# Performance work log

Hardware: AMD Instinct MI355X
Metric: run time of the kernel (lower is better)

Reference implementation:

```python
import jax, jax.numpy as jnp
import numpy as np

TOPK = 2


def setup_inputs() -> dict:
    key = jax.random.key(0)
    k1, k2, k3, k4, k5 = jax.random.split(key, 5)
    D, H, E = 1024, 1408, 8
    hidden_states = jax.random.normal(k1, (2, 1024, D), dtype=jnp.float32)
    gate_w = jax.random.normal(k2, (E, D), dtype=jnp.float32) * 0.02
    w1g = jax.random.normal(k3, (E, D, H), dtype=jnp.float32) * 0.02
    w1u = jax.random.normal(k4, (E, D, H), dtype=jnp.float32) * 0.02
    w2 = jax.random.normal(k5, (E, H, D), dtype=jnp.float32) * 0.02
    return {"hidden_states": hidden_states, "gate_w": gate_w, "w1g": w1g, "w1u": w1u, "w2": w2}


def reference(hidden_states, gate_w, w1g, w1u, w2):
    # hidden_states: [B, S, D]; expert weights: w1g/w1u [E, D, H], w2 [E, H, D]
    B, S, D = hidden_states.shape
    E = gate_w.shape[0]
    x = hidden_states.reshape(-1, D)  # [T, D]
    T = x.shape[0]

    # --- MoEGate: softmax scores, top-k routing (no topk renorm) ---
    logits = x @ gate_w.T                      # [T, E]
    scores = jax.nn.softmax(logits, axis=-1)   # [T, E]
    topk_w, topk_idx = jax.lax.top_k(scores, TOPK)  # [T, K]

    # Per-token combine coefficient for each expert: coeff[t, e] = sum_k w[t,k] * (idx[t,k]==e)
    coeff = jnp.zeros((T, E), dtype=x.dtype).at[jnp.arange(T)[:, None], topk_idx].add(topk_w)

    # --- Grouped expert MLP (swiglu): identical math to permute + grouped GEMM + unpermute ---
    g = jnp.einsum('td,edh->teh', x, w1g)      # [T, E, H]
    u = jnp.einsum('td,edh->teh', x, w1u)      # [T, E, H]
    h = jax.nn.silu(g) * u                     # [T, E, H]
    y = jnp.einsum('teh,te,ehd->td', h, coeff, w2)  # [T, D]
    return y.reshape(B, S, D)
```

## Files before the change

### kernel.cpp

```cpp
#include <hip/hip_runtime.h>

#define TOK 2048
#define DDIM 1024
#define HDIM 1408
#define ENUM 8
#define NSLOT (2 * TOK)
#define UP_NB 22
#define UP_KS 32
#define DN_NB 16
#define DN_KS 44
#define DN_KH 22
#define TC_W1_BLK 2816
#define TC_ALL_BLK 4224

typedef unsigned int uint;
typedef unsigned short ushort;

using bf16x8 = __attribute__((ext_vector_type(8))) __bf16;
using f32x4  = __attribute__((ext_vector_type(4))) float;

__device__ __forceinline__ float silu_f(float g) {
    return g / (1.0f + __expf(-g));
}

__device__ __forceinline__ ushort cvt_bf16(float f) {
    uint u = __float_as_uint(f);
    u += 0x7FFFu + ((u >> 16) & 1u);
    return (ushort)(u >> 16);
}

__device__ __forceinline__ void gl2lds16(const void* g, void* l) {
    __builtin_amdgcn_global_load_lds(
        (const __attribute__((address_space(1))) uint*)g,
        (__attribute__((address_space(3))) uint*)l, 16, 0, 0);
}

__global__ __launch_bounds__(64) void gate1_kernel(
    const float* __restrict__ x, const float* __restrict__ gw,
    int* __restrict__ tinfo, float* __restrict__ wslot, ushort* __restrict__ xb)
{
    const int t = blockIdx.x;
    const int lane = threadIdx.x;
    const float* xr = x + (size_t)t * DDIM;
    ushort* xbr = xb + (size_t)t * DDIM;
    float xv[16];
#pragma unroll
    for (int i = 0; i < 16; ++i) xv[i] = xr[lane + 64 * i];
#pragma unroll
    for (int i = 0; i < 16; ++i) xbr[lane + 64 * i] = cvt_bf16(xv[i]);
    float logit[ENUM];
#pragma unroll
    for (int e = 0; e < ENUM; ++e) {
        const float* gr = gw + (size_t)e * DDIM;
        float acc = 0.f;
#pragma unroll
        for (int i = 0; i < 16; ++i) acc += xv[i] * gr[lane + 64 * i];
#pragma unroll
        for (int s = 32; s > 0; s >>= 1) acc += __shfl_xor(acc, s, 64);
        logit[e] = acc;
    }
    if (lane == 0) {
        float mx = logit[0];
#pragma unroll
        for (int e = 1; e < ENUM; ++e) mx = fmaxf(mx, logit[e]);
        float p[ENUM]; float se = 0.f;
#pragma unroll
        for (int e = 0; e < ENUM; ++e) { p[e] = __expf(logit[e] - mx); se += p[e]; }
        float inv = 1.0f / se;
#pragma unroll
        for (int e = 0; e < ENUM; ++e) p[e] *= inv;
        int i0 = 0;
#pragma unroll
        for (int e = 1; e < ENUM; ++e) if (p[e] > p[i0]) i0 = e;
        int i1 = (i0 == 0) ? 1 : 0;
#pragma unroll
        for (int e = 0; e < ENUM; ++e) if (e != i0 && p[e] > p[i1]) i1 = e;
        tinfo[t] = i0 | (i1 << 4);
        wslot[(t << 1)] = p[i0];
        wslot[(t << 1) | 1] = p[i1];
    }
}

__global__ __launch_bounds__(256) void tcast_all_kernel(
    const float* __restrict__ w1g, const float* __restrict__ w1u,
    const float* __restrict__ w2, ushort* __restrict__ BgP,
    ushort* __restrict__ BuP, ushort* __restrict__ W2P,
    const int* __restrict__ tinfo, int* __restrict__ counts,
    int* __restrict__ toks)
{
    const int bid = blockIdx.x;
    const int tid = threadIdx.x;

    __shared__ float Ls[32][69];
    __shared__ int cnt;

    if (bid >= TC_ALL_BLK) {
        const int e = bid - TC_ALL_BLK;
        if (tid == 0) cnt = 0;
        __syncthreads();
        for (int t = tid; t < TOK; t += 256) {
            int info = tinfo[t];
            if ((info & 15) == e) { int p = atomicAdd(&cnt, 1); toks[e * TOK + p] = (t << 1); }
            if ((info >> 4) == e) { int p = atomicAdd(&cnt, 1); toks[e * TOK + p] = (t << 1) | 1; }
        }
        __syncthreads();
        if (tid == 0) counts[e] = cnt;
        return;
    }

    const float* src; ushort* dst; int N, KS, NB, e, nb, ks0;
    if (bid < TC_W1_BLK) {
        const int z = bid / 176;
        const int rem = bid - z * 176;
        src = (z & 8) ? w1u : w1g;
        dst = (z & 8) ? BuP : BgP;
        N = HDIM; KS = UP_KS; NB = UP_NB; e = z & 7;
        nb = rem >> 3; ks0 = (rem & 7) * 4;
    } else {
        const int b2 = bid - TC_W1_BLK;
        e = b2 / 176;
        const int rem = b2 - e * 176;
        src = w2; dst = W2P;
        N = DDIM; KS = DN_KS; NB = DN_NB;
        nb = rem / 11; ks0 = (rem - nb * 11) * 4;
    }

    const int n4 = (tid & 15) * 4;
    const int nn = tid >> 2;
    const int kk0 = (tid & 3) * 8;

    for (int ksi = 0; ksi < 4; ++ksi) {
        const int ks = ks0 + ksi;
        const float* st = src + (size_t)e * ((size_t)KS * 32) * N + (size_t)(ks * 32) * N + nb * 64;
#pragma unroll
        for (int r = 0; r < 2; ++r) {
            int k = (tid >> 4) + r * 16;
            float4 v = *(const float4*)(st + (size_t)k * N + n4);
            Ls[k][n4 + 0] = v.x; Ls[k][n4 + 1] = v.y; Ls[k][n4 + 2] = v.z; Ls[k][n4 + 3] = v.w;
        }
        __syncthreads();
        ushort* dt = dst + ((((size_t)e * NB + nb) * KS) + ks) * 2048;
        ushort o[8];
#pragma unroll
        for (int j = 0; j < 8; ++j) o[j] = cvt_bf16(Ls[kk0 + j][nn]);
        *(uint4*)(dt + nn * 32 + kk0) = *(uint4*)o;
        __syncthreads();
    }
}

__global__ __launch_bounds__(256, 4) void up_mfma(
    const ushort* __restrict__ xb, const ushort* __restrict__ BgP,
    const ushort* __restrict__ BuP, const int* __restrict__ counts,
    const int* __restrict__ toks, ushort* __restrict__ Hbuf)
{
    const int e = blockIdx.z;
    const int cnt = counts[e];
    const int m0 = blockIdx.y * 128;
    if (m0 >= cnt) return;
    const int nb = blockIdx.x;
    const int tid = threadIdx.x;
    const int w = tid >> 6;
    const int lane = tid & 63;
    const int q = lane >> 4;
    const int l15 = lane & 15;
    const int wr = w >> 1;
    const int wc = w & 1;

    __shared__ ushort As[2][128][32];
    __shared__ ushort Bgs[2][64][32];
    __shared__ ushort Bus[2][64][32];
    __shared__ int rowslot[128];

    if (tid < 128) rowslot[tid] = (m0 + tid < cnt) ? toks[e * TOK + m0 + tid] : -1;
    __syncthreads();

    const int srow = w * 16 + (lane >> 2);
    const int clog = (((lane & 3) + 4 - ((srow >> 1) & 3)) & 3) * 8;
    const int as0 = rowslot[srow];
    const int as1 = rowslot[srow + 64];
    const ushort* agp0 = xb + (size_t)(as0 < 0 ? 0 : (as0 >> 1)) * DDIM + clog;
    const ushort* agp1 = xb + (size_t)(as1 < 0 ? 0 : (as1 >> 1)) * DDIM + clog;
    const size_t tb = (size_t)(e * UP_NB + nb) * UP_KS * 2048;
    const ushort* bgp = BgP + tb + srow * 32 + clog;
    const ushort* bup = BuP + tb + srow * 32 + clog;

    const int coff = ((q + (l15 >> 1)) & 3) * 8;

    f32x4 accg[4][2], accu[4][2];
#pragma unroll
    for (int i = 0; i < 4; ++i)
#pragma unroll
        for (int j = 0; j < 2; ++j) { accg[i][j] = (f32x4)0.f; accu[i][j] = (f32x4)0.f; }

#define UP_PREFETCH(KSV, B)                                        \
    {                                                              \
        gl2lds16(agp0 + (KSV) * 32, &As[B][w * 16][0]);            \
        gl2lds16(agp1 + (KSV) * 32, &As[B][64 + w * 16][0]);       \
        gl2lds16(bgp + (size_t)(KSV) * 2048, &Bgs[B][w * 16][0]);  \
        gl2lds16(bup + (size_t)(KSV) * 2048, &Bus[B][w * 16][0]);  \
    }

    UP_PREFETCH(0, 0);
    __syncthreads();

    for (int ks = 0; ks < UP_KS; ++ks) {
        const int cur = ks & 1;
        const int nxt = cur ^ 1;
        if (ks + 1 < UP_KS) UP_PREFETCH(ks + 1, nxt);

        bf16x8 a[4], bg[2], bu[2];
#pragma unroll
        for (int mi = 0; mi < 4; ++mi)
            a[mi] = *(const bf16x8*)&As[cur][wr * 64 + mi * 16 + l15][coff];
#pragma unroll
        for (int ni = 0; ni < 2; ++ni) {
            bg[ni] = *(const bf16x8*)&Bgs[cur][wc * 32 + ni * 16 + l15][coff];
            bu[ni] = *(const bf16x8*)&Bus[cur][wc * 32 + ni * 16 + l15][coff];
        }
#pragma unroll
        for (int mi = 0; mi < 4; ++mi)
#pragma unroll
            for (int ni = 0; ni < 2; ++ni) {
                accg[mi][ni] = __builtin_amdgcn_mfma_f32_16x16x32_bf16(a[mi], bg[ni], accg[mi][ni], 0, 0, 0);
                accu[mi][ni] = __builtin_amdgcn_mfma_f32_16x16x32_bf16(a[mi], bu[ni], accu[mi][ni], 0, 0, 0);
            }
        __syncthreads();
    }
#undef UP_PREFETCH

#pragma unroll
    for (int mi = 0; mi < 4; ++mi) {
#pragma unroll
        for (int r = 0; r < 4; ++r) {
            int ml = wr * 64 + mi * 16 + q * 4 + r;
            int slot = rowslot[ml];
            if (slot < 0) continue;
            ushort* hrow = Hbuf + (size_t)slot * HDIM + nb * 64 + wc * 32 + l15;
#pragma unroll
            for (int ni = 0; ni < 2; ++ni)
                hrow[ni * 16] = cvt_bf16(silu_f(accg[mi][ni][r]) * accu[mi][ni][r]);
        }
    }
}

__global__ __launch_bounds__(256, 4) void down_mfma(
    const ushort* __restrict__ Hbuf, const ushort* __restrict__ W2P,
    const int* __restrict__ counts, const int* __restrict__ toks,
    float* __restrict__ Ybuf)
{
    const int z = blockIdx.z;
    const int e = z >> 1;
    const int kh = z & 1;
    const int cnt = counts[e];
    const int m0 = blockIdx.y * 128;
    if (m0 >= cnt) return;
    const int nb = blockIdx.x;
    const int tid = threadIdx.x;
    const int w = tid >> 6;
    const int lane = tid & 63;
    const int q = lane >> 4;
    const int l15 = lane & 15;
    const int wr = w >> 1;
    const int wc = w & 1;

    __shared__ ushort As[2][128][32];
    __shared__ ushort Bs[2][128][32];
    __shared__ int rowslot[128];

    if (tid < 128) rowslot[tid] = (m0 + tid < cnt) ? toks[e * TOK + m0 + tid] : -1;
    __syncthreads();

    const int srow = w * 16 + (lane >> 2);
    const int clog = (((lane & 3) + 4 - ((srow >> 1) & 3)) & 3) * 8;
    const int as0 = rowslot[srow];
    const int as1 = rowslot[srow + 64];
    const ushort* agp0 = Hbuf + (size_t)(as0 < 0 ? 0 : as0) * HDIM + kh * (DN_KH * 32) + clog;
    const ushort* agp1 = Hbuf + (size_t)(as1 < 0 ? 0 : as1) * HDIM + kh * (DN_KH * 32) + clog;
    const int nb2 = nb * 2;
    const ushort* bp0 = W2P + ((size_t)(e * DN_NB + nb2) * DN_KS + kh * DN_KH) * 2048 + srow * 32 + clog;
    const ushort* bp1 = W2P + ((size_t)(e * DN_NB + nb2 + 1) * DN_KS + kh * DN_KH) * 2048 + srow * 32 + clog;

    const int coff = ((q + (l15 >> 1)) & 3) * 8;

    f32x4 acc[4][4];
#pragma unroll
    for (int i = 0; i < 4; ++i)
#pragma unroll
        for (int j = 0; j < 4; ++j) acc[i][j] = (f32x4)0.f;

#define DN_PREFETCH(KSV, B)                                           \
    {                                                                 \
        gl2lds16(agp0 + (KSV) * 32, &As[B][w * 16][0]);               \
        gl2lds16(agp1 + (KSV) * 32, &As[B][64 + w * 16][0]);          \
        gl2lds16(bp0 + (size_t)(KSV) * 2048, &Bs[B][w * 16][0]);      \
        gl2lds16(bp1 + (size_t)(KSV) * 2048, &Bs[B][64 + w * 16][0]); \
    }

    DN_PREFETCH(0, 0);
    __syncthreads();

    for (int ks = 0; ks < DN_KH; ++ks) {
        const int cur = ks & 1;
        const int nxt = cur ^ 1;
        if (ks + 1 < DN_KH) DN_PREFETCH(ks + 1, nxt);

        bf16x8 a[4], b[4];
#pragma unroll
        for (int mi = 0; mi < 4; ++mi)
            a[mi] = *(const bf16x8*)&As[cur][wr * 64 + mi * 16 + l15][coff];
#pragma unroll
        for (int ni = 0; ni < 4; ++ni)
            b[ni] = *(const bf16x8*)&Bs[cur][wc * 64 + ni * 16 + l15][coff];
#pragma unroll
        for (int mi = 0; mi < 4; ++mi)
#pragma unroll
            for (int ni = 0; ni < 4; ++ni)
                acc[mi][ni] = __builtin_amdgcn_mfma_f32_16x16x32_bf16(a[mi], b[ni], acc[mi][ni], 0, 0, 0);
        __syncthreads();
    }
#undef DN_PREFETCH

    float* Yp = Ybuf + (size_t)kh * NSLOT * DDIM;
#pragma unroll
    for (int mi = 0; mi < 4; ++mi) {
#pragma unroll
        for (int r = 0; r < 4; ++r) {
            int ml = wr * 64 + mi * 16 + q * 4 + r;
            int slot = rowslot[ml];
            if (slot < 0) continue;
            float* yr = Yp + (size_t)slot * DDIM + nb * 128 + wc * 64 + l15;
#pragma unroll
            for (int ni = 0; ni < 4; ++ni)
                yr[ni * 16] = acc[mi][ni][r];
        }
    }
}

__global__ __launch_bounds__(256) void combine_kernel(
    const float* __restrict__ Ybuf, const float* __restrict__ wslot,
    float* __restrict__ y)
{
    const int t = blockIdx.x;
    const int j = threadIdx.x * 4;
    const float w0 = wslot[2 * t];
    const float w1 = wslot[2 * t + 1];
    const float* y00 = Ybuf + ((size_t)2 * t) * DDIM + j;
    const float* y01 = Ybuf + ((size_t)2 * t + 1) * DDIM + j;
    const float* y10 = y00 + (size_t)NSLOT * DDIM;
    const float* y11 = y01 + (size_t)NSLOT * DDIM;
    float4 a0 = *(const float4*)y00;
    float4 b0 = *(const float4*)y01;
    float4 a1 = *(const float4*)y10;
    float4 b1 = *(const float4*)y11;
    float4 o;
    o.x = w0 * (a0.x + a1.x) + w1 * (b0.x + b1.x);
    o.y = w0 * (a0.y + a1.y) + w1 * (b0.y + b1.y);
    o.z = w0 * (a0.z + a1.z) + w1 * (b0.z + b1.z);
    o.w = w0 * (a0.w + a1.w) + w1 * (b0.w + b1.w);
    *(float4*)(y + (size_t)t * DDIM + j) = o;
}

extern "C" void kernel_launch(void* const* d_in, const int* in_sizes, int n_in,
                              void* d_out, int out_size, void* d_ws, size_t ws_size,
                              hipStream_t stream) {
    const float* x   = (const float*)d_in[0];
    const float* gw  = (const float*)d_in[1];
    const float* w1g = (const float*)d_in[2];
    const float* w1u = (const float*)d_in[3];
    const float* w2  = (const float*)d_in[4];
    float* y = (float*)d_out;
    char* ws = (char*)d_ws;

    size_t off = 0;
    int*    counts = (int*)(ws + off);   off += 256;
    int*    toks   = (int*)(ws + off);   off += (size_t)ENUM * TOK * 4;
    float*  wslot  = (float*)(ws + off); off += (size_t)NSLOT * 4;
    int*    tinfo  = (int*)(ws + off);   off += (size_t)TOK * 4;
    off = (off + 255) & ~(size_t)255;
    ushort* xb     = (ushort*)(ws + off); off += (size_t)TOK * DDIM * 2;
    size_t regA = off;
    ushort* BgP  = (ushort*)(ws + regA);
    ushort* BuP  = (ushort*)(ws + regA + (size_t)ENUM * DDIM * HDIM * 2);
    float*  Ybuf = (float*)(ws + regA);
    off = regA + (size_t)2 * ENUM * DDIM * HDIM * 2;
    ushort* W2P  = (ushort*)(ws + off);  off += (size_t)ENUM * HDIM * DDIM * 2;
    ushort* Hbuf = (ushort*)(ws + off);

    gate1_kernel<<<TOK, 64, 0, stream>>>(x, gw, tinfo, wslot, xb);
    tcast_all_kernel<<<TC_ALL_BLK + ENUM, 256, 0, stream>>>(
        w1g, w1u, w2, BgP, BuP, W2P, tinfo, counts, toks);

    up_mfma<<<dim3(UP_NB, TOK / 128, ENUM), 256, 0, stream>>>(xb, BgP, BuP, counts, toks, Hbuf);
    down_mfma<<<dim3(DDIM / 128, TOK / 128, 16), 256, 0, stream>>>(Hbuf, W2P, counts, toks, Ybuf);
    combine_kernel<<<TOK, 256, 0, stream>>>(Ybuf, wslot, y);
}
```

Measured before the change: 259.7 us.

## Fuse gate softmax into weight-cast kernel and use wave-ballot routing scatter

Moves the gate/softmax/top-k work into the same launch as the weight transpose-cast, so gating runs concurrently with weight conversion instead of as a separate preceding kernel. The weight cast drops its LDS staging and barriers, reading strided columns directly into registers and writing packed bf16. The token-to-expert scatter becomes its own small kernel using wavefront ballots with one atomic per wave. Direct strided loads may coalesce less well than the previous float4 row loads, and the order of tokens within each expert list can change.

```diff
diff --git a/kernel.cpp b/kernel.cpp
--- a/kernel.cpp
+++ b/kernel.cpp
@@ -12,9 +12,11 @@
 #define DN_KH 22
 #define TC_W1_BLK 2816
 #define TC_ALL_BLK 4224
+#define GATE_BLK 512
 
 typedef unsigned int uint;
 typedef unsigned short ushort;
+typedef unsigned long long ull;
 
 using bf16x8 = __attribute__((ext_vector_type(8))) __bf16;
 using f32x4  = __attribute__((ext_vector_type(4))) float;
@@ -35,12 +37,53 @@
         (__attribute__((address_space(3))) uint*)l, 16, 0, 0);
 }
 
-__global__ __launch_bounds__(64) void gate1_kernel(
+__global__ __launch_bounds__(256) void tcast_gate_kernel(
+    const float* __restrict__ w1g, const float* __restrict__ w1u,
+    const float* __restrict__ w2, ushort* __restrict__ BgP,
+    ushort* __restrict__ BuP, ushort* __restrict__ W2P,
     const float* __restrict__ x, const float* __restrict__ gw,
     int* __restrict__ tinfo, float* __restrict__ wslot, ushort* __restrict__ xb)
 {
-    const int t = blockIdx.x;
-    const int lane = threadIdx.x;
+    const int bid = blockIdx.x;
+    const int tid = threadIdx.x;
+
+    if (bid < TC_ALL_BLK) {
+        const float* src; ushort* dst; int N, KS, NB, e, nb, ks0;
+        if (bid < TC_W1_BLK) {
+            const int z = bid / 176;
+            const int rem = bid - z * 176;
+            src = (z & 8) ? w1u : w1g;
+            dst = (z & 8) ? BuP : BgP;
+            N = HDIM; KS = UP_KS; NB = UP_NB; e = z & 7;
+            nb = rem >> 3; ks0 = (rem & 7) * 4;
+        } else {
+            const int b2 = bid - TC_W1_BLK;
+            e = b2 / 176;
+            const int rem = b2 - e * 176;
+            src = w2; dst = W2P;
+            N = DDIM; KS = DN_KS; NB = DN_NB;
+            nb = rem / 11; ks0 = (rem - nb * 11) * 4;
+        }
+        const int kg = tid & 3;
+        const int nn = tid >> 2;
+        const float* sb = src + (size_t)e * ((size_t)KS * 32) * N + nb * 64 + nn;
+        ushort* db = dst + ((((size_t)e * NB + nb) * KS) + ks0) * 2048 + nn * 32 + kg * 8;
+#pragma unroll
+        for (int ksi = 0; ksi < 4; ++ksi) {
+            const float* st = sb + (size_t)((ks0 + ksi) * 32 + kg * 8) * N;
+            float v[8];
+#pragma unroll
+            for (int j = 0; j < 8; ++j) v[j] = st[(size_t)j * N];
+            ushort o[8];
+#pragma unroll
+            for (int j = 0; j < 8; ++j) o[j] = cvt_bf16(v[j]);
+            *(uint4*)(db + ksi * 2048) = *(uint4*)o;
+        }
+        return;
+    }
+
+    const int t = (bid - TC_ALL_BLK) * 4 + (tid >> 6);
+    const int lane = tid & 63;
     const float* xr = x + (size_t)t * DDIM;
     ushort* xbr = xb + (size_t)t * DDIM;
     float xv[16];
@@ -81,71 +124,37 @@
     }
 }
 
-__global__ __launch_bounds__(256) void tcast_all_kernel(
-    const float* __restrict__ w1g, const float* __restrict__ w1u,
-    const float* __restrict__ w2, ushort* __restrict__ BgP,
-    ushort* __restrict__ BuP, ushort* __restrict__ W2P,
-    const int* __restrict__ tinfo, int* __restrict__ counts,
-    int* __restrict__ toks)
+__global__ __launch_bounds__(256) void gate2_kernel(
+    const int* __restrict__ tinfo, int* __restrict__ counts, int* __restrict__ toks)
 {
-    const int bid = blockIdx.x;
+    const int e = blockIdx.x;
     const int tid = threadIdx.x;
-
-    __shared__ float Ls[32][69];
+    const int lane = tid & 63;
     __shared__ int cnt;
-
-    if (bid >= TC_ALL_BLK) {
-        const int e = bid - TC_ALL_BLK;
-        if (tid == 0) cnt = 0;
-        __syncthreads();
-        for (int t = tid; t < TOK; t += 256) {
-            int info = tinfo[t];
-            if ((info & 15) == e) { int p = atomicAdd(&cnt, 1); toks[e * TOK + p] = (t << 1); }
-            if ((info >> 4) == e) { int p = atomicAdd(&cnt, 1); toks[e * TOK + p] = (t << 1) | 1; }
-        }
-        __syncthreads();
-        if (tid == 0) counts[e] = cnt;
-        return;
-    }
-
-    const float* src; ushort* dst; int N, KS, NB, e, nb, ks0;
-    if (bid < TC_W1_BLK) {
-        const int z = bid / 176;
-        const int rem = bid - z * 176;
-        src = (z & 8) ? w1u : w1g;
-        dst = (z & 8) ? BuP : BgP;
-        N = HDIM; KS = UP_KS; NB = UP_NB; e = z & 7;
-        nb = rem >> 3; ks0 = (rem & 7) * 4;
-    } else {
-        const int b2 = bid - TC_W1_BLK;
-        e = b2 / 176;
-        const int rem = b2 - e * 176;
-        src = w2; dst = W2P;
-        N = DDIM; KS = DN_KS; NB = DN_NB;
-        nb = rem / 11; ks0 = (rem - nb * 11) * 4;
-    }
-
-    const int n4 = (tid & 15) * 4;
-    const int nn = tid >> 2;
-    const int kk0 = (tid & 3) * 8;
-
-    for (int ksi = 0; ksi < 4; ++ksi) {
-        const int ks = ks0 + ksi;
-        const float* st = src + (size_t)e * ((size_t)KS * 32) * N + (size_t)(ks * 32) * N + nb * 64;
-#pragma unroll
-        for (int r = 0; r < 2; ++r) {
-            int k = (tid >> 4) + r * 16;
-            float4 v = *(const float4*)(st + (size_t)k * N + n4);
-            Ls[k][n4 + 0] = v.x; Ls[k][n4 + 1] = v.y; Ls[k][n4 + 2] = v.z; Ls[k][n4 + 3] = v.w;
-        }
-        __syncthreads();
-        ushort* dt = dst + ((((size_t)e * NB + nb) * KS) + ks) * 2048;
-        ushort o[8];
-#pragma unroll
-        for (int j = 0; j < 8; ++j) o[j] = cvt_bf16(Ls[kk0 + j][nn]);
-        *(uint4*)(dt + nn * 32 + kk0) = *(uint4*)o;
-        __syncthreads();
-    }
+    if (tid == 0) cnt = 0;
+    __syncthreads();
+    int* te = toks + e * TOK;
+    for (int t = tid; t < TOK; t += 256) {
+        int info = tinfo[t];
+        ull m0 = __ballot((info & 15) == e);
+        if (m0) {
+            int base;
+            if (lane == 0) base = atomicAdd(&cnt, __popcll(m0));
+            base = __shfl(base, 0, 64);
+            if ((m0 >> lane) & 1)
+                te[base + __popcll(m0 & ((1ull << lane) - 1))] = (t << 1);
+        }
+        ull m1 = __ballot((info >> 4) == e);
+        if (m1) {
+            int base;
+            if (lane == 0) base = atomicAdd(&cnt, __popcll(m1));
+            base = __shfl(base, 0, 64);
+            if ((m1 >> lane) & 1)
+                te[base + __popcll(m1 & ((1ull << lane) - 1))] = (t << 1) | 1;
+        }
+    }
+    __syncthreads();
+    if (tid == 0) counts[e] = cnt;
 }
 
 __global__ __launch_bounds__(256, 4) void up_mfma(
@@ -386,9 +395,9 @@
     ushort* W2P  = (ushort*)(ws + off);  off += (size_t)ENUM * HDIM * DDIM * 2;
     ushort* Hbuf = (ushort*)(ws + off);
 
-    gate1_kernel<<<TOK, 64, 0, stream>>>(x, gw, tinfo, wslot, xb);
-    tcast_all_kernel<<<TC_ALL_BLK + ENUM, 256, 0, stream>>>(
-        w1g, w1u, w2, BgP, BuP, W2P, tinfo, counts, toks);
+    tcast_gate_kernel<<<TC_ALL_BLK + GATE_BLK, 256, 0, stream>>>(
+        w1g, w1u, w2, BgP, BuP, W2P, x, gw, tinfo, wslot, xb);
+    gate2_kernel<<<ENUM, 256, 0, stream>>>(tinfo, counts, toks);
 
     up_mfma<<<dim3(UP_NB, TOK / 128, ENUM), 256, 0, stream>>>(xb, BgP, BuP, counts, toks, Hbuf);
     down_mfma<<<dim3(DDIM / 128, TOK / 128, 16), 256, 0, stream>>>(Hbuf, W2P, counts, toks, Ybuf);
```

Measured after the change: 256.2 us. About the same (-1.4%).
